# Kernel optimization log

Hardware: AMD Instinct MI355X
Metric: run time of the kernel (lower is better)

The kernel has to match this reference:

```python
import jax, jax.numpy as jnp
import numpy as np

B, S = 128, 512
VOCAB, E, H, T = 100000, 100, 128, 10  # tagset_size=10 -> CRF over T-1=9 tags
HD = H // 2  # per-direction LSTM hidden


def setup_inputs():
    key = jax.random.key(0)
    ks = jax.random.split(key, 14)
    s = 0.08
    inputs = jax.random.randint(ks[0], (B, S), 1, VOCAB)
    tags = jax.random.randint(ks[1], (B, S), 1, T)  # valid after tags-1 shift
    mask = jnp.ones((B, S), dtype=bool)
    emb = (jax.random.normal(ks[2], (VOCAB, E)) * s).at[0].set(0.0)  # padding_idx=0 row zeroed
    Wih_f = jax.random.normal(ks[3], (4 * HD, E)) * s
    Whh_f = jax.random.normal(ks[4], (4 * HD, HD)) * s
    b_f = jax.random.normal(ks[5], (4 * HD,)) * s
    Wih_b = jax.random.normal(ks[6], (4 * HD, E)) * s
    Whh_b = jax.random.normal(ks[7], (4 * HD, HD)) * s
    b_b = jax.random.normal(ks[8], (4 * HD,)) * s
    W_out = jax.random.normal(ks[9], (T, H)) * s
    b_out = jax.random.normal(ks[10], (T,)) * s
    start = jax.random.normal(ks[11], (T - 1,)) * s
    end = jax.random.normal(ks[12], (T - 1,)) * s
    trans = jax.random.normal(ks[13], (T - 1, T - 1)) * s
    return dict(inputs=inputs, tags=tags, mask=mask, emb=emb,
                Wih_f=Wih_f, Whh_f=Whh_f, b_f=b_f,
                Wih_b=Wih_b, Whh_b=Whh_b, b_b=b_b,
                W_out=W_out, b_out=b_out, start=start, end=end, trans=trans)


def _lstm_dir(x, Wih, Whh, b, reverse):
    # x: [S, B, E] time-major; PyTorch gate order i,f,g,o; b = b_ih + b_hh
    h0 = jnp.zeros((x.shape[1], Whh.shape[1]), x.dtype)

    def step(carry, xt):
        h, c = carry
        gates = xt @ Wih.T + h @ Whh.T + b
        i, f, g, o = jnp.split(gates, 4, axis=-1)
        c = jax.nn.sigmoid(f) * c + jax.nn.sigmoid(i) * jnp.tanh(g)
        h = jax.nn.sigmoid(o) * jnp.tanh(c)
        return (h, c), h

    _, hs = jax.lax.scan(step, (h0, h0), x, reverse=reverse)
    return hs  # [S, B, HD]


def _crf_nll(em, tags, mask, start, end, trans):
    # Linear-chain CRF (torchcrf-style). em: [S,B,K], tags/mask: [S,B]
    pick = lambda e, t: jnp.take_along_axis(e, t[:, None], axis=-1)[:, 0]
    # numerator: score of the gold path
    score0 = start[tags[0]] + pick(em[0], tags[0])

    def num_step(sc, inp):
        em_t, t, tp, m = inp
        return sc + jnp.where(m, trans[tp, t] + pick(em_t, t), 0.0), None

    score, _ = jax.lax.scan(num_step, score0, (em[1:], tags[1:], tags[:-1], mask[1:]))
    last_idx = mask.sum(0).astype(jnp.int32) - 1
    last_tags = jnp.take_along_axis(tags, last_idx[None, :], axis=0)[0]
    score = score + end[last_tags]
    # denominator: forward algorithm (log partition)
    alpha0 = start[None, :] + em[0]  # [B,K]

    def fwd_step(alpha, inp):
        em_t, m = inp
        nxt = jax.nn.logsumexp(alpha[:, :, None] + trans[None, :, :] + em_t[:, None, :], axis=1)
        return jnp.where(m[:, None], nxt, alpha), None

    alpha, _ = jax.lax.scan(fwd_step, alpha0, (em[1:], mask[1:]))
    logZ = jax.nn.logsumexp(alpha + end[None, :], axis=1)
    return -(score - logZ).mean()  # loss = -log_likelihood.mean()


def _forward(inputs, tags, mask, emb, Wih_f, Whh_f, b_f, Wih_b, Whh_b, b_b, W_out, b_out, start, end, trans):
    x = emb[inputs].transpose(1, 0, 2)  # [S,B,E]
    h = jnp.concatenate([_lstm_dir(x, Wih_f, Whh_f, b_f, False),
                         _lstm_dir(x, Wih_b, Whh_b, b_b, True)], axis=-1)  # [S,B,H]
    # dropout is identity at eval; slice off tag 0 as in the module
    em = (h @ W_out.T + b_out)[:, :, 1:]  # [S,B,T-1]
    return _crf_nll(em, (tags - 1).T, mask.T, start, end, trans)


def reference(inputs, tags, mask, emb, Wih_f, Whh_f, b_f, Wih_b, Whh_b, b_b, W_out, b_out, start, end, trans):
    return _forward(inputs, tags, mask, emb, Wih_f, Whh_f, b_f, Wih_b, Whh_b, b_b, W_out, b_out, start, end, trans)
```

## Files before the change

### kernel.cpp

```cpp
#include <hip/hip_runtime.h>
#include <math.h>

#define SB 512
#define NB 128
#define HD 64

typedef _Float16 h2 __attribute__((ext_vector_type(2)));
typedef _Float16 f16x8 __attribute__((ext_vector_type(8)));
typedef float f32x4 __attribute__((ext_vector_type(4)));
union U4 { uint4 u; h2 h[4]; _Float16 f[8]; };
union UF { uint4 u; f16x8 h8; _Float16 f[8]; };
union U2 { uint2 u; _Float16 f[4]; };
union UH { unsigned u; _Float16 f[2]; };

__device__ __forceinline__ float frcp(float x) { return __builtin_amdgcn_rcpf(x); }
__device__ __forceinline__ float fsig(float x) { return frcp(1.0f + __expf(-x)); }
__device__ __forceinline__ float ftanh(float x) {
    float t = __expf(-2.0f * fabsf(x));
    float r = (1.0f - t) * frcp(1.0f + t);
    return copysignf(r, x);
}
__device__ __forceinline__ float fdot2(h2 a, h2 b, float c) {
    return __builtin_amdgcn_fdot2(a, b, c, false);
}

__global__ void prep_kernel(const float* __restrict__ Wih_f, const float* __restrict__ Wih_bb,
                            const float* __restrict__ Whh_f, const float* __restrict__ Whh_bb,
                            const float* __restrict__ b_f, const float* __restrict__ b_bb,
                            const float* __restrict__ trans,
                            unsigned* __restrict__ W2h, unsigned* __restrict__ whh16,
                            float* __restrict__ bias2, float* __restrict__ Eexp)
{
    int idx = blockIdx.x * 256 + threadIdx.x;
    if (idx < 32768) {
        int col = idx >> 6, d = idx & 63;
        int dir = col >> 8, r = col & 255, j = r >> 2, g = r & 3;
        const float* src = (dir ? Wih_bb : Wih_f) + (g * 64 + j) * 100;
        UH u; u.u = 0;
        if (d < 50) { u.f[0] = (_Float16)src[2 * d]; u.f[1] = (_Float16)src[2 * d + 1]; }
        W2h[idx] = u.u;
    } else if (idx < 49152) {
        int d = idx - 32768;
        int kp = d & 31, u = (d >> 5) & 63, g = (d >> 11) & 3, dir = d >> 13;
        const float* src = (dir ? Whh_bb : Whh_f) + (g * 64 + u) * 64 + 2 * kp;
        UH uu; uu.f[0] = (_Float16)src[0]; uu.f[1] = (_Float16)src[1];
        int k4 = kp >> 2, q = kp & 3;
        whh16[(((dir * 4 + g) * 8 + k4) * 64 + u) * 4 + q] = uu.u;
    } else if (idx < 49664) {
        int col = idx - 49152;
        int dir = col >> 8, r = col & 255, j = r >> 2, g = r & 3;
        bias2[col] = (dir ? b_bb : b_f)[g * 64 + j];
    } else if (idx < 49745) {
        int i = idx - 49664;
        Eexp[i] = __expf(trans[i]);
    }
}

__global__ __launch_bounds__(256, 2) void gemm_kernel(
    const int* __restrict__ inputs, const float* __restrict__ emb,
    const unsigned* __restrict__ W2h, const float* __restrict__ bias2,
    _Float16* __restrict__ xgh)
{
    __shared__ __align__(16) unsigned sE[128 * 64];
    __shared__ __align__(16) unsigned sW[128 * 64];
    __shared__ float sbias[512];
    __shared__ int stok[128];
    const int tt = blockIdx.x;
    const int tid = threadIdx.x;
    const int w = tid >> 6, l = tid & 63;
    const int q = l >> 4, n = l & 15;

    if (tid < 128) stok[tid] = inputs[tid * SB + tt];
    for (int i = tid; i < 512; i += 256) sbias[i] = bias2[i];
    __syncthreads();
    for (int idx = tid; idx < 8192; idx += 256) {
        int row = idx >> 6, d = idx & 63;
        unsigned v = 0;
        if (d < 50) {
            const float* ep = emb + (size_t)stok[row] * 100 + 2 * d;
            UH u; u.f[0] = (_Float16)ep[0]; u.f[1] = (_Float16)ep[1];
            v = u.u;
        }
        sE[idx] = v;
    }

    for (int cg = 0; cg < 4; ++cg) {
        __syncthreads();
        for (int idx = tid; idx < 2048; idx += 256)
            ((uint4*)sW)[idx] = ((const uint4*)W2h)[cg * 2048 + idx];
        __syncthreads();

        f32x4 acc[2][8];
        #pragma unroll
        for (int m = 0; m < 2; ++m)
            #pragma unroll
            for (int c = 0; c < 8; ++c)
                #pragma unroll
                for (int r = 0; r < 4; ++r) acc[m][c][r] = 0.f;

        #pragma unroll
        for (int kt = 0; kt < 4; ++kt) {
            const int ko = 16 * kt + 2 * q;
            UF A0, A1;
            {
                const unsigned* rp = &sE[(16 * (2 * w + 0) + n) * 64 + ko];
                uint2 lo = *(const uint2*)rp;
                uint2 hi = *(const uint2*)(rp + 8);
                A0.u = make_uint4(lo.x, lo.y, hi.x, hi.y);
                rp = &sE[(16 * (2 * w + 1) + n) * 64 + ko];
                lo = *(const uint2*)rp;
                hi = *(const uint2*)(rp + 8);
                A1.u = make_uint4(lo.x, lo.y, hi.x, hi.y);
            }
            UF B[8];
            #pragma unroll
            for (int c = 0; c < 8; ++c) {
                const unsigned* rp = &sW[(16 * c + n) * 64 + ko];
                uint2 lo = *(const uint2*)rp;
                uint2 hi = *(const uint2*)(rp + 8);
                B[c].u = make_uint4(lo.x, lo.y, hi.x, hi.y);
            }
            #pragma unroll
            for (int c = 0; c < 8; ++c) {
                acc[0][c] = __builtin_amdgcn_mfma_f32_16x16x32_f16(A0.h8, B[c].h8, acc[0][c], 0, 0, 0);
                acc[1][c] = __builtin_amdgcn_mfma_f32_16x16x32_f16(A1.h8, B[c].h8, acc[1][c], 0, 0, 0);
            }
        }

        #pragma unroll
        for (int m = 0; m < 2; ++m)
            #pragma unroll
            for (int c = 0; c < 8; ++c) {
                int col = cg * 128 + 16 * c + n;
                float bc = sbias[col];
                #pragma unroll
                for (int r = 0; r < 4; ++r) {
                    int row = 16 * (2 * w + m) + 4 * q + r;
                    xgh[(size_t)(tt * NB + row) * 512 + col] = (_Float16)(acc[m][c][r] + bc);
                }
            }
    }
}

__global__ __attribute__((amdgpu_flat_work_group_size(64, 64), amdgpu_waves_per_eu(1, 1)))
void lstm_kernel(
    const _Float16* __restrict__ xgh, const unsigned* __restrict__ whh16,
    _Float16* __restrict__ h16)
{
    const int blk = blockIdx.x;
    const int b = blk & (NB - 1);
    const int dir = blk >> 7;
    const int j = threadIdx.x;

    __shared__ __align__(16) unsigned wlds[8192];
    __shared__ __align__(16) _Float16 hbuf[64];

    {
        const uint4* src = (const uint4*)(whh16 + dir * 8192);
        uint4* dst = (uint4*)wlds;
        #pragma unroll
        for (int i = 0; i < 32; ++i) dst[i * 64 + j] = src[i * 64 + j];
    }
    hbuf[j] = (_Float16)0.f;
    float c = 0.f;

    const int t0 = dir ? (SB - 1) : 0;
    const ptrdiff_t xstride = (dir ? -1 : 1) * (ptrdiff_t)(NB * 512);
    const _Float16* xp = xgh + ((size_t)(t0 * NB + b)) * 512 + dir * 256 + j * 4;
    _Float16* hp = h16 + ((size_t)(b * 2 + dir) * SB + t0) * 64 + j;
    const ptrdiff_t hstride = (dir ? -1 : 1) * (ptrdiff_t)64;

    U2 p0, p1, p2;
    p0.u = *(const uint2*)xp;
    p1.u = *(const uint2*)(xp + xstride);
    p2.u = *(const uint2*)(xp + 2 * xstride);
    const _Float16* xq = xp + 3 * xstride;

    const uint4* wl = (const uint4*)wlds;

    for (int s = 0; s < SB; ++s) {
        float a0 = (float)p0.f[0], a1 = (float)p0.f[1];
        float a2 = (float)p0.f[2], a3 = (float)p0.f[3];
        p0 = p1; p1 = p2;
        p2.u = *(const uint2*)xq;
        xq += xstride;

        U4 hv[8];
        #pragma unroll
        for (int k4 = 0; k4 < 8; ++k4) hv[k4].u = *(const uint4*)&hbuf[k4 * 8];

        float g0[4] = {a0, 0.f, 0.f, 0.f};
        float g1[4] = {a1, 0.f, 0.f, 0.f};
        float g2[4] = {a2, 0.f, 0.f, 0.f};
        float g3[4] = {a3, 0.f, 0.f, 0.f};
        #pragma unroll
        for (int k4 = 0; k4 < 8; ++k4) {
            U4 w0, w1, w2, w3;
            w0.u = wl[(0 * 8 + k4) * 64 + j];
            w1.u = wl[(1 * 8 + k4) * 64 + j];
            w2.u = wl[(2 * 8 + k4) * 64 + j];
            w3.u = wl[(3 * 8 + k4) * 64 + j];
            const int p = k4 & 3;
            #pragma unroll
            for (int q = 0; q < 4; ++q) {
                g0[p] = fdot2(hv[k4].h[q], w0.h[q], g0[p]);
                g1[p] = fdot2(hv[k4].h[q], w1.h[q], g1[p]);
                g2[p] = fdot2(hv[k4].h[q], w2.h[q], g2[p]);
                g3[p] = fdot2(hv[k4].h[q], w3.h[q], g3[p]);
            }
        }
        a0 = (g0[0] + g0[1]) + (g0[2] + g0[3]);
        a1 = (g1[0] + g1[1]) + (g1[2] + g1[3]);
        a2 = (g2[0] + g2[1]) + (g2[2] + g2[3]);
        a3 = (g3[0] + g3[1]) + (g3[2] + g3[3]);

        float ig = fsig(a0), fg = fsig(a1), gg = ftanh(a2), og = fsig(a3);
        c = fg * c + ig * gg;
        float h = og * ftanh(c);
        *hp = (_Float16)h;
        hp += hstride;
        hbuf[j] = (_Float16)h;
    }
}

__global__ __launch_bounds__(256, 1) void proj_kernel(
    const _Float16* __restrict__ h16, const float* __restrict__ W_out,
    const float* __restrict__ b_out, float* __restrict__ em3)
{
    __shared__ __align__(16) unsigned tile[128 * 64];
    __shared__ __align__(16) unsigned sWo[9 * 64];
    __shared__ float sb[9];
    const int b = blockIdx.x, tid = threadIdx.x;

    for (int i2 = tid; i2 < 576; i2 += 256) {
        int k = i2 >> 6, jp = i2 & 63;
        const float* src = W_out + (k + 1) * 128 + 2 * jp;
        UH u; u.f[0] = (_Float16)src[0]; u.f[1] = (_Float16)src[1];
        sWo[i2] = u.u;
    }
    if (tid < 9) sb[tid] = b_out[1 + tid];

    float* dst0 = em3 + (size_t)b * (SB * 12);

    for (int tt = 0; tt < 4; ++tt) {
        const int t0 = tt * 128;
        __syncthreads();
        #pragma unroll
        for (int dir = 0; dir < 2; ++dir) {
            const unsigned* src = (const unsigned*)(h16 + ((size_t)(b * 2 + dir) * SB + t0) * 64);
            for (int i = tid; i < 4096; i += 256) {
                int t = i >> 5, jp = i & 31;
                tile[t * 64 + dir * 32 + jp] = src[i];
            }
        }
        __syncthreads();

        for (int o = tid; o < 1152; o += 256) {
            int tl = o / 9, k = o - 9 * tl;
            const U4* hr = (const U4*)&tile[tl * 64];
            const U4* wr = (const U4*)&sWo[k * 64];
            float pa = 0.f, pb = 0.f;
            #pragma unroll
            for (int qq = 0; qq < 16; qq += 2) {
                U4 hv = hr[qq], wv = wr[qq];
                U4 hv2 = hr[qq + 1], wv2 = wr[qq + 1];
                #pragma unroll
                for (int z = 0; z < 4; ++z) {
                    pa = fdot2(hv.h[z], wv.h[z], pa);
                    pb = fdot2(hv2.h[z], wv2.h[z], pb);
                }
            }
            dst0[(t0 + tl) * 12 + k] = pa + pb + sb[k];
        }
    }
}

__global__ __launch_bounds__(64, 1) void crf_gold(
    const float* __restrict__ em3, const int* __restrict__ tags,
    const float* __restrict__ startv, const float* __restrict__ endv,
    const float* __restrict__ trans, float* __restrict__ gold)
{
    const int b = blockIdx.x, l = threadIdx.x;
    const int* tb = tags + (size_t)b * SB;
    const float* eb = em3 + (size_t)b * (SB * 12);
    float sc = 0.f;
    for (int t = l; t < SB; t += 64) {
        int tg = tb[t] - 1;
        if (t > 0) {
            int tp = tb[t - 1] - 1;
            sc += trans[tp * 9 + tg] + eb[t * 12 + tg];
        }
    }
    if (l == 0) {
        int tg0 = tb[0] - 1, tgl = tb[SB - 1] - 1;
        sc += startv[tg0] + eb[tg0] + endv[tgl];
    }
    #pragma unroll
    for (int off = 32; off > 0; off >>= 1) sc += __shfl_down(sc, off);
    if (l == 0) gold[b] = sc;
}

__global__ __launch_bounds__(256, 1) void crf_scan(
    const float* __restrict__ em3, const float* __restrict__ Eexp,
    float* __restrict__ Pws)
{
    const int lane = blockIdx.x * 256 + threadIdx.x;
    const int c = lane & 31, b = lane >> 5;

    float E[81];
    #pragma unroll
    for (int i = 0; i < 81; ++i) E[i] = Eexp[i];

    float P[81];
    #pragma unroll
    for (int i = 0; i < 81; ++i) P[i] = 0.f;
    #pragma unroll
    for (int i = 0; i < 9; ++i) P[i * 9 + i] = 1.f;
    float M = 0.f;

    const int t0 = 1 + 16 * c;
    const int nst = (t0 + 16 <= SB) ? 16 : (SB - t0);
    const float* ep = em3 + (size_t)b * (SB * 12) + t0 * 12;

    for (int s = 0; s < nst; ++s, ep += 12) {
        float4 e0 = *(const float4*)ep;
        float4 e1 = *(const float4*)(ep + 4);
        float e8 = ep[8];
        float ex[9] = { __expf(e0.x), __expf(e0.y), __expf(e0.z), __expf(e0.w),
                        __expf(e1.x), __expf(e1.y), __expf(e1.z), __expf(e1.w),
                        __expf(e8) };
        #pragma unroll
        for (int i = 0; i < 9; ++i) {
            float tmp[9];
            #pragma unroll
            for (int jj = 0; jj < 9; ++jj) tmp[jj] = P[i * 9] * E[jj];
            #pragma unroll
            for (int k = 1; k < 9; ++k)
                #pragma unroll
                for (int jj = 0; jj < 9; ++jj) tmp[jj] += P[i * 9 + k] * E[k * 9 + jj];
            #pragma unroll
            for (int jj = 0; jj < 9; ++jj) P[i * 9 + jj] = tmp[jj] * ex[jj];
        }
        if ((s & 3) == 3) {
            float mx = P[0];
            #pragma unroll
            for (int i = 1; i < 81; ++i) mx = fmaxf(mx, P[i]);
            M += __logf(mx);
            float r = frcp(mx);
            #pragma unroll
            for (int i = 0; i < 81; ++i) P[i] *= r;
        }
    }

    float* dst = Pws + (size_t)lane * 84;
    #pragma unroll
    for (int i = 0; i < 81; ++i) dst[i] = P[i];
    dst[81] = M;
}

__global__ __launch_bounds__(128, 1) void crf_combine(
    const float* __restrict__ em3, const float* __restrict__ Pws,
    const float* __restrict__ gold, const float* __restrict__ startv,
    const float* __restrict__ endv, float* __restrict__ out)
{
    const int b = threadIdx.x;
    float A[9], M = 0.f;
    {
        const float* eb = em3 + (size_t)b * (SB * 12);
        float4 e0 = *(const float4*)eb;
        float4 e1 = *(const float4*)(eb + 4);
        float e[9] = { e0.x, e0.y, e0.z, e0.w, e1.x, e1.y, e1.z, e1.w, eb[8] };
        #pragma unroll
        for (int k = 0; k < 9; ++k) A[k] = __expf(startv[k] + e[k]);
    }

    for (int c = 0; c < 32; ++c) {
        const float4* src = (const float4*)(Pws + ((size_t)b * 32 + c) * 84);
        float buf[84];
        #pragma unroll
        for (int qq = 0; qq < 21; ++qq) {
            float4 v = src[qq];
            buf[4 * qq] = v.x; buf[4 * qq + 1] = v.y; buf[4 * qq + 2] = v.z; buf[4 * qq + 3] = v.w;
        }
        float tmp[9];
        #pragma unroll
        for (int jj = 0; jj < 9; ++jj) tmp[jj] = A[0] * buf[jj];
        #pragma unroll
        for (int i = 1; i < 9; ++i)
            #pragma unroll
            for (int jj = 0; jj < 9; ++jj) tmp[jj] += A[i] * buf[i * 9 + jj];
        float mx = tmp[0];
        #pragma unroll
        for (int jj = 1; jj < 9; ++jj) mx = fmaxf(mx, tmp[jj]);
        M += __logf(mx) + buf[81];
        float r = frcp(mx);
        #pragma unroll
        for (int jj = 0; jj < 9; ++jj) A[jj] = tmp[jj] * r;
    }

    float Z = 0.f;
    #pragma unroll
    for (int k = 0; k < 9; ++k) Z += A[k] * __expf(endv[k]);
    float part = M + __logf(Z) - gold[b];

    #pragma unroll
    for (int off = 32; off > 0; off >>= 1) part += __shfl_down(part, off);
    __shared__ float sm[2];
    if ((b & 63) == 0) sm[b >> 6] = part;
    __syncthreads();
    if (b == 0) out[0] = (sm[0] + sm[1]) * (1.0f / NB);
}

extern "C" void kernel_launch(void* const* d_in, const int* in_sizes, int n_in,
                              void* d_out, int out_size, void* d_ws, size_t ws_size,
                              hipStream_t stream)
{
    const int*   inputs = (const int*)d_in[0];
    const int*   tags   = (const int*)d_in[1];
    const float* emb    = (const float*)d_in[3];
    const float* Wih_f  = (const float*)d_in[4];
    const float* Whh_f  = (const float*)d_in[5];
    const float* b_f    = (const float*)d_in[6];
    const float* Wih_b  = (const float*)d_in[7];
    const float* Whh_b  = (const float*)d_in[8];
    const float* b_b    = (const float*)d_in[9];
    const float* W_out  = (const float*)d_in[10];
    const float* b_out  = (const float*)d_in[11];
    const float* startv = (const float*)d_in[12];
    const float* endv   = (const float*)d_in[13];
    const float* transv = (const float*)d_in[14];

    char* w = (char*)d_ws;
    float* em3     = (float*)w;     w += (size_t)NB * SB * 12 * 4;
    _Float16* xgh  = (_Float16*)w;  w += (size_t)SB * NB * 512 * 2;
    _Float16* h16  = (_Float16*)w;  w += (size_t)NB * 2 * SB * 64 * 2;
    float* Pws     = (float*)w;     w += (size_t)NB * 32 * 84 * 4;
    float* gold    = (float*)w;     w += NB * 4;
    unsigned* W2h  = (unsigned*)w;  w += 32768 * 4;
    unsigned* whh16= (unsigned*)w;  w += 16384 * 4;
    float* bias2   = (float*)w;     w += 512 * 4;
    float* Eexp    = (float*)w;     w += 81 * 4;

    prep_kernel<<<195, 256, 0, stream>>>(Wih_f, Wih_b, Whh_f, Whh_b, b_f, b_b, transv,
                                         W2h, whh16, bias2, Eexp);
    gemm_kernel<<<SB, 256, 0, stream>>>(inputs, emb, W2h, bias2, xgh);
    lstm_kernel<<<256, 64, 0, stream>>>(xgh, whh16, h16);
    proj_kernel<<<NB, 256, 0, stream>>>(h16, W_out, b_out, em3);
    crf_gold<<<NB, 64, 0, stream>>>(em3, tags, startv, endv, transv, gold);
    crf_scan<<<16, 256, 0, stream>>>(em3, Eexp, Pws);
    crf_combine<<<1, 128, 0, stream>>>(em3, Pws, gold, startv, endv, (float*)d_out);
}
```

Measured before the change: 547.4 us.

## Fuse projection with CRF gold and scan kernels; pad gemm LDS rows

Merges the output projection, gold-path scoring and chunked CRF forward scan into one per-batch kernel that keeps emissions in shared memory. Only the first timestep's emissions are written to global for the combine step. It also pads the shared-memory rows of the input GEMM to reduce bank conflicts. This removes two kernel launches and the global round trip of the emission tensor, but the CRF scan now runs on only 32 lanes per block behind the projection.

```diff
diff --git a/kernel.cpp b/kernel.cpp
--- a/kernel.cpp
+++ b/kernel.cpp
@@ -61,8 +61,8 @@
     const unsigned* __restrict__ W2h, const float* __restrict__ bias2,
     _Float16* __restrict__ xgh)
 {
-    __shared__ __align__(16) unsigned sE[128 * 64];
-    __shared__ __align__(16) unsigned sW[128 * 64];
+    __shared__ __align__(16) unsigned sE[128 * 68];
+    __shared__ __align__(16) unsigned sW[128 * 68];
     __shared__ float sbias[512];
     __shared__ int stok[128];
     const int tt = blockIdx.x;
@@ -81,13 +81,13 @@
             UH u; u.f[0] = (_Float16)ep[0]; u.f[1] = (_Float16)ep[1];
             v = u.u;
         }
-        sE[idx] = v;
+        sE[row * 68 + d] = v;
     }
 
     for (int cg = 0; cg < 4; ++cg) {
         __syncthreads();
         for (int idx = tid; idx < 2048; idx += 256)
-            ((uint4*)sW)[idx] = ((const uint4*)W2h)[cg * 2048 + idx];
+            ((uint4*)sW)[(idx >> 4) * 17 + (idx & 15)] = ((const uint4*)W2h)[cg * 2048 + idx];
         __syncthreads();
 
         f32x4 acc[2][8];
@@ -103,11 +103,11 @@
             const int ko = 16 * kt + 2 * q;
             UF A0, A1;
             {
-                const unsigned* rp = &sE[(16 * (2 * w + 0) + n) * 64 + ko];
+                const unsigned* rp = &sE[(16 * (2 * w + 0) + n) * 68 + ko];
                 uint2 lo = *(const uint2*)rp;
                 uint2 hi = *(const uint2*)(rp + 8);
                 A0.u = make_uint4(lo.x, lo.y, hi.x, hi.y);
-                rp = &sE[(16 * (2 * w + 1) + n) * 64 + ko];
+                rp = &sE[(16 * (2 * w + 1) + n) * 68 + ko];
                 lo = *(const uint2*)rp;
                 hi = *(const uint2*)(rp + 8);
                 A1.u = make_uint4(lo.x, lo.y, hi.x, hi.y);
@@ -115,7 +115,7 @@
             UF B[8];
             #pragma unroll
             for (int c = 0; c < 8; ++c) {
-                const unsigned* rp = &sW[(16 * c + n) * 64 + ko];
+                const unsigned* rp = &sW[(16 * c + n) * 68 + ko];
                 uint2 lo = *(const uint2*)rp;
                 uint2 hi = *(const uint2*)(rp + 8);
                 B[c].u = make_uint4(lo.x, lo.y, hi.x, hi.y);
@@ -223,11 +223,15 @@
     }
 }
 
-__global__ __launch_bounds__(256, 1) void proj_kernel(
+__global__ __launch_bounds__(256, 1) void pgs_kernel(
     const _Float16* __restrict__ h16, const float* __restrict__ W_out,
-    const float* __restrict__ b_out, float* __restrict__ em3)
+    const float* __restrict__ b_out, const int* __restrict__ tags,
+    const float* __restrict__ startv, const float* __restrict__ endv,
+    const float* __restrict__ trans, const float* __restrict__ Eexp,
+    float* __restrict__ em0, float* __restrict__ gold, float* __restrict__ Pws)
 {
     __shared__ __align__(16) unsigned tile[128 * 64];
+    __shared__ __align__(16) float em3L[SB * 12];
     __shared__ __align__(16) unsigned sWo[9 * 64];
     __shared__ float sb[9];
     const int b = blockIdx.x, tid = threadIdx.x;
@@ -240,8 +244,6 @@
     }
     if (tid < 9) sb[tid] = b_out[1 + tid];
 
-    float* dst0 = em3 + (size_t)b * (SB * 12);
-
     for (int tt = 0; tt < 4; ++tt) {
         const int t0 = tt * 128;
         __syncthreads();
@@ -270,103 +272,97 @@
                     pb = fdot2(hv2.h[z], wv2.h[z], pb);
                 }
             }
-            dst0[(t0 + tl) * 12 + k] = pa + pb + sb[k];
-        }
-    }
-}
-
-__global__ __launch_bounds__(64, 1) void crf_gold(
-    const float* __restrict__ em3, const int* __restrict__ tags,
-    const float* __restrict__ startv, const float* __restrict__ endv,
-    const float* __restrict__ trans, float* __restrict__ gold)
-{
-    const int b = blockIdx.x, l = threadIdx.x;
-    const int* tb = tags + (size_t)b * SB;
-    const float* eb = em3 + (size_t)b * (SB * 12);
-    float sc = 0.f;
-    for (int t = l; t < SB; t += 64) {
-        int tg = tb[t] - 1;
-        if (t > 0) {
-            int tp = tb[t - 1] - 1;
-            sc += trans[tp * 9 + tg] + eb[t * 12 + tg];
-        }
-    }
-    if (l == 0) {
-        int tg0 = tb[0] - 1, tgl = tb[SB - 1] - 1;
-        sc += startv[tg0] + eb[tg0] + endv[tgl];
-    }
-    #pragma unroll
-    for (int off = 32; off > 0; off >>= 1) sc += __shfl_down(sc, off);
-    if (l == 0) gold[b] = sc;
-}
-
-__global__ __launch_bounds__(256, 1) void crf_scan(
-    const float* __restrict__ em3, const float* __restrict__ Eexp,
-    float* __restrict__ Pws)
-{
-    const int lane = blockIdx.x * 256 + threadIdx.x;
-    const int c = lane & 31, b = lane >> 5;
-
-    float E[81];
-    #pragma unroll
-    for (int i = 0; i < 81; ++i) E[i] = Eexp[i];
-
-    float P[81];
-    #pragma unroll
-    for (int i = 0; i < 81; ++i) P[i] = 0.f;
-    #pragma unroll
-    for (int i = 0; i < 9; ++i) P[i * 9 + i] = 1.f;
-    float M = 0.f;
-
-    const int t0 = 1 + 16 * c;
-    const int nst = (t0 + 16 <= SB) ? 16 : (SB - t0);
-    const float* ep = em3 + (size_t)b * (SB * 12) + t0 * 12;
-
-    for (int s = 0; s < nst; ++s, ep += 12) {
-        float4 e0 = *(const float4*)ep;
-        float4 e1 = *(const float4*)(ep + 4);
-        float e8 = ep[8];
-        float ex[9] = { __expf(e0.x), __expf(e0.y), __expf(e0.z), __expf(e0.w),
-                        __expf(e1.x), __expf(e1.y), __expf(e1.z), __expf(e1.w),
-                        __expf(e8) };
-        #pragma unroll
-        for (int i = 0; i < 9; ++i) {
-            float tmp[9];
-            #pragma unroll
-            for (int jj = 0; jj < 9; ++jj) tmp[jj] = P[i * 9] * E[jj];
-            #pragma unroll
-            for (int k = 1; k < 9; ++k)
-                #pragma unroll
-                for (int jj = 0; jj < 9; ++jj) tmp[jj] += P[i * 9 + k] * E[k * 9 + jj];
-            #pragma unroll
-            for (int jj = 0; jj < 9; ++jj) P[i * 9 + jj] = tmp[jj] * ex[jj];
-        }
-        if ((s & 3) == 3) {
-            float mx = P[0];
-            #pragma unroll
-            for (int i = 1; i < 81; ++i) mx = fmaxf(mx, P[i]);
-            M += __logf(mx);
-            float r = frcp(mx);
-            #pragma unroll
-            for (int i = 0; i < 81; ++i) P[i] *= r;
-        }
-    }
-
-    float* dst = Pws + (size_t)lane * 84;
-    #pragma unroll
-    for (int i = 0; i < 81; ++i) dst[i] = P[i];
-    dst[81] = M;
+            em3L[(t0 + tl) * 12 + k] = pa + pb + sb[k];
+        }
+    }
+    __syncthreads();
+
+    if (tid >= 128 && tid < 137)
+        em0[b * 12 + (tid - 128)] = em3L[tid - 128];
+
+    if (tid >= 64 && tid < 128) {
+        const int l = tid - 64;
+        const int* tb = tags + (size_t)b * SB;
+        float sc = 0.f;
+        for (int t = l; t < SB; t += 64) {
+            int tg = tb[t] - 1;
+            if (t > 0) {
+                int tp = tb[t - 1] - 1;
+                sc += trans[tp * 9 + tg] + em3L[t * 12 + tg];
+            }
+        }
+        if (l == 0) {
+            int tg0 = tb[0] - 1, tgl = tb[SB - 1] - 1;
+            sc += startv[tg0] + em3L[tg0] + endv[tgl];
+        }
+        #pragma unroll
+        for (int off = 32; off > 0; off >>= 1) sc += __shfl_down(sc, off);
+        if (l == 0) gold[b] = sc;
+    }
+
+    if (tid < 32) {
+        const int c = tid;
+        float E[81];
+        #pragma unroll
+        for (int i = 0; i < 81; ++i) E[i] = Eexp[i];
+
+        float P[81];
+        #pragma unroll
+        for (int i = 0; i < 81; ++i) P[i] = 0.f;
+        #pragma unroll
+        for (int i = 0; i < 9; ++i) P[i * 9 + i] = 1.f;
+        float M = 0.f;
+
+        const int t0 = 1 + 16 * c;
+        const int nst = (t0 + 16 <= SB) ? 16 : (SB - t0);
+        const float* ep = &em3L[t0 * 12];
+
+        for (int s = 0; s < nst; ++s, ep += 12) {
+            float4 e0 = *(const float4*)ep;
+            float4 e1 = *(const float4*)(ep + 4);
+            float e8 = ep[8];
+            float ex[9] = { __expf(e0.x), __expf(e0.y), __expf(e0.z), __expf(e0.w),
+                            __expf(e1.x), __expf(e1.y), __expf(e1.z), __expf(e1.w),
+                            __expf(e8) };
+            #pragma unroll
+            for (int i = 0; i < 9; ++i) {
+                float tmp[9];
+                #pragma unroll
+                for (int jj = 0; jj < 9; ++jj) tmp[jj] = P[i * 9] * E[jj];
+                #pragma unroll
+                for (int k = 1; k < 9; ++k)
+                    #pragma unroll
+                    for (int jj = 0; jj < 9; ++jj) tmp[jj] += P[i * 9 + k] * E[k * 9 + jj];
+                #pragma unroll
+                for (int jj = 0; jj < 9; ++jj) P[i * 9 + jj] = tmp[jj] * ex[jj];
+            }
+            if ((s & 3) == 3) {
+                float mx = P[0];
+                #pragma unroll
+                for (int i = 1; i < 81; ++i) mx = fmaxf(mx, P[i]);
+                M += __logf(mx);
+                float r = frcp(mx);
+                #pragma unroll
+                for (int i = 0; i < 81; ++i) P[i] *= r;
+            }
+        }
+
+        float* dst = Pws + ((size_t)b * 32 + c) * 84;
+        #pragma unroll
+        for (int i = 0; i < 81; ++i) dst[i] = P[i];
+        dst[81] = M;
+    }
 }
 
 __global__ __launch_bounds__(128, 1) void crf_combine(
-    const float* __restrict__ em3, const float* __restrict__ Pws,
+    const float* __restrict__ em0, const float* __restrict__ Pws,
     const float* __restrict__ gold, const float* __restrict__ startv,
     const float* __restrict__ endv, float* __restrict__ out)
 {
     const int b = threadIdx.x;
     float A[9], M = 0.f;
     {
-        const float* eb = em3 + (size_t)b * (SB * 12);
+        const float* eb = em0 + (size_t)b * 12;
         float4 e0 = *(const float4*)eb;
         float4 e1 = *(const float4*)(eb + 4);
         float e[9] = { e0.x, e0.y, e0.z, e0.w, e1.x, e1.y, e1.z, e1.w, eb[8] };
@@ -431,7 +427,7 @@
     const float* transv = (const float*)d_in[14];
 
     char* w = (char*)d_ws;
-    float* em3     = (float*)w;     w += (size_t)NB * SB * 12 * 4;
+    float* em0     = (float*)w;     w += (size_t)NB * SB * 12 * 4;
     _Float16* xgh  = (_Float16*)w;  w += (size_t)SB * NB * 512 * 2;
     _Float16* h16  = (_Float16*)w;  w += (size_t)NB * 2 * SB * 64 * 2;
     float* Pws     = (float*)w;     w += (size_t)NB * 32 * 84 * 4;
@@ -445,8 +441,7 @@
                                          W2h, whh16, bias2, Eexp);
     gemm_kernel<<<SB, 256, 0, stream>>>(inputs, emb, W2h, bias2, xgh);
     lstm_kernel<<<256, 64, 0, stream>>>(xgh, whh16, h16);
-    proj_kernel<<<NB, 256, 0, stream>>>(h16, W_out, b_out, em3);
-    crf_gold<<<NB, 64, 0, stream>>>(em3, tags, startv, endv, transv, gold);
-    crf_scan<<<16, 256, 0, stream>>>(em3, Eexp, Pws);
-    crf_combine<<<1, 128, 0, stream>>>(em3, Pws, gold, startv, endv, (float*)d_out);
-}
+    pgs_kernel<<<NB, 256, 0, stream>>>(h16, W_out, b_out, tags, startv, endv, transv,
+                                       Eexp, em0, gold, Pws);
+    crf_combine<<<1, 128, 0, stream>>>(em0, Pws, gold, startv, endv, (float*)d_out);
+}
```

After: 487.1 us. 11.0% less time.
